# Performance work log

Hardware: AMD Instinct MI355X
Metric: run time of the kernel (lower is better)

Reference implementation:

```python
import jax, jax.numpy as jnp
import numpy as np

N, E, H = 4096, 32768, 8
D0, C1, C2, C3 = 256, 448, 384, 256
K, M, G = 4, 500, 2000
NEG = 0.2   # GATConv LeakyReLU negative slope
EPS = 1e-5  # LayerNorm eps


def _gat(x, src, dst, W, a_s, a_d, b, heads, out_ch, concat):
    # PyG GATConv (self-loops already appended to src/dst by caller).
    n = x.shape[0]
    xp = (x @ W).reshape(n, heads, out_ch)                 # [N,H,C]
    s = jnp.einsum('nhc,hc->nh', xp, a_s)                  # alpha_src per node
    d = jnp.einsum('nhc,hc->nh', xp, a_d)                  # alpha_dst per node
    e = jax.nn.leaky_relu(s[src] + d[dst], NEG)            # [E,H]
    m = jax.ops.segment_max(e, dst, num_segments=n)
    m = jnp.where(jnp.isfinite(m), m, 0.0)
    p = jnp.exp(e - m[dst])
    z = jax.ops.segment_sum(p, dst, num_segments=n)
    alpha = p / (z[dst] + 1e-16)                           # per-dst softmax
    out = jax.ops.segment_sum(alpha[:, :, None] * xp[src], dst, num_segments=n)
    out = out.reshape(n, heads * out_ch) if concat else out[:, 0, :]
    return out + b


def _ln(x, g, b):
    mu = x.mean(-1, keepdims=True)
    v = ((x - mu) ** 2).mean(-1, keepdims=True)
    return (x - mu) * jax.lax.rsqrt(v + EPS) * g + b


def setup_inputs() -> dict:
    key = jax.random.key(0)
    ks = jax.random.split(key, 20)
    sc = 0.05
    inp = {
        'x': jax.random.normal(ks[0], (N, D0), jnp.float32),
        'edge_index': jax.random.randint(ks[1], (2, E), 0, N, jnp.int32),
        'W1': jax.random.normal(ks[2], (D0, H * C1), jnp.float32) * sc,
        'as1': jax.random.normal(ks[3], (H, C1), jnp.float32) * sc,
        'ad1': jax.random.normal(ks[4], (H, C1), jnp.float32) * sc,
        'b1': jnp.zeros((H * C1,), jnp.float32),
        'g1': jnp.ones((H * C1,), jnp.float32),
        'be1': jnp.zeros((H * C1,), jnp.float32),
        'W2': jax.random.normal(ks[5], (H * C1, H * C2), jnp.float32) * sc,
        'as2': jax.random.normal(ks[6], (H, C2), jnp.float32) * sc,
        'ad2': jax.random.normal(ks[7], (H, C2), jnp.float32) * sc,
        'b2': jnp.zeros((H * C2,), jnp.float32),
        'g2': jnp.ones((H * C2,), jnp.float32),
        'be2': jnp.zeros((H * C2,), jnp.float32),
        'W3': jax.random.normal(ks[8], (H * C2, H * C3), jnp.float32) * sc,
        'as3': jax.random.normal(ks[9], (H, C3), jnp.float32) * sc,
        'ad3': jax.random.normal(ks[10], (H, C3), jnp.float32) * sc,
        'b3': jnp.zeros((H * C3,), jnp.float32),
        'g3': jnp.ones((H * C3,), jnp.float32),
        'be3': jnp.zeros((H * C3,), jnp.float32),
        'Wh': jax.random.normal(ks[11], (K, H * C3, M), jnp.float32) * sc,
        'ash': jax.random.normal(ks[12], (K, 1, M), jnp.float32) * sc,
        'adh': jax.random.normal(ks[13], (K, 1, M), jnp.float32) * sc,
        'bh': jnp.zeros((K, M), jnp.float32),
        'idx': jnp.arange(G, dtype=jnp.int32).reshape(K, M),
    }
    return inp


def reference(x, edge_index, W1, as1, ad1, b1, g1, be1, W2, as2, ad2, b2, g2, be2,
              W3, as3, ad3, b3, g3, be3, Wh, ash, adh, bh, idx):
    n = x.shape[0]
    # eval mode: dropout_edge is identity; PyG GATConv adds self-loops
    loops = jnp.arange(n, dtype=edge_index.dtype)
    src = jnp.concatenate([edge_index[0], loops])
    dst = jnp.concatenate([edge_index[1], loops])

    h = jax.nn.relu(_gat(x, src, dst, W1, as1, ad1, b1, H, C1, True))
    h = _ln(h, g1, be1)
    h = jax.nn.relu(_gat(h, src, dst, W2, as2, ad2, b2, H, C2, True))
    h = _ln(h, g2, be2)
    h = jax.nn.relu(_gat(h, src, dst, W3, as3, ad3, b3, H, C3, True))
    h = _ln(h, g3, be3)

    per_head = jax.vmap(
        lambda Wk, ak_s, ak_d, bk: _gat(h, src, dst, Wk, ak_s, ak_d, bk, 1, M, False)
    )(Wh, ash, adh, bh)                                    # [K,N,M]

    vals = per_head.transpose(1, 0, 2).reshape(n, K * M)   # [N, G] in head order
    full = jnp.zeros((n, G), vals.dtype).at[:, idx.reshape(-1)].set(vals)
    return full, per_head
```

## Files before the change

### kernel.cpp

```cpp
#include <hip/hip_runtime.h>

#define NN 4096
#define EE 32768
#define ETOT (EE + NN)
#define HH 8
#define KK 4
#define MM 500
#define GG 2000
#define NEGS 0.2f
#define LNEPS 1e-5f

typedef unsigned short ushort;
typedef _Float16 half_t;
typedef __attribute__((ext_vector_type(8))) _Float16 half8;
typedef __attribute__((ext_vector_type(4))) _Float16 half4;
typedef __attribute__((ext_vector_type(4))) float floatx4;


__device__ __forceinline__ void get_edge(const int* __restrict__ ei, int e, int& s, int& d) {
    if (e < EE) { s = ei[e]; d = ei[EE + e]; }
    else        { s = e - EE; d = e - EE; }
}

__device__ __forceinline__ half_t f2h(float x) { return (half_t)x; }

__device__ __forceinline__ void async_lds16(const half_t* g, half_t* l) {
    __builtin_amdgcn_global_load_lds(
        (const __attribute__((address_space(1))) unsigned int*)(const void*)g,
        (__attribute__((address_space(3))) unsigned int*)(void*)l,
        16, 0, 0);
}


__global__ void k_count(const int* __restrict__ ei, int* deg) {
    int e = blockIdx.x * 256 + threadIdx.x;
    if (e < ETOT) { int s, d; get_edge(ei, e, s, d); atomicAdd(&deg[d], 1); }
}

__global__ void k_scan(int* deg, int* rs, int n) {
    __shared__ int sums[1024];
    int tid = threadIdx.x;
    int base = tid * 4;
    int loc[4]; int s = 0;
    #pragma unroll
    for (int i = 0; i < 4; i++) {
        int v = (base + i < n) ? deg[base + i] : 0;
        loc[i] = s; s += v;
    }
    #pragma unroll
    for (int i = 0; i < 4; i++)
        if (base + i < n) deg[base + i] = 0;
    sums[tid] = s;
    __syncthreads();
    for (int off = 1; off < 1024; off <<= 1) {
        int v = (tid >= off) ? sums[tid - off] : 0;
        __syncthreads();
        sums[tid] += v;
        __syncthreads();
    }
    int prev = (tid > 0) ? sums[tid - 1] : 0;
    #pragma unroll
    for (int i = 0; i < 4; i++)
        if (base + i < n) rs[base + i] = prev + loc[i];
    if (tid == 1023) rs[n] = sums[1023];
}

__global__ void k_fill_f2h(const int* __restrict__ ei, const int* __restrict__ rs,
                           int* cur, int* csr_src,
                           const floatx4* __restrict__ x4, half4* __restrict__ xh4) {
    int i = blockIdx.x * 256 + threadIdx.x;
    if (i < ETOT) {
        int s, d; get_edge(ei, i, s, d);
        int pos = rs[d] + atomicAdd(&cur[d], 1);
        csr_src[pos] = s;
    }
    if (i < NN * 64) {
        floatx4 v = x4[i];
        half4 o;
        o[0] = f2h(v[0]); o[1] = f2h(v[1]); o[2] = f2h(v[2]); o[3] = f2h(v[3]);
        xh4[i] = o;
    }
}


__device__ __forceinline__ void sd_body(const half_t* __restrict__ xp,
                                        const float* __restrict__ as_,
                                        const float* __restrict__ ad_,
                                        float* s, float* d, int H, int C,
                                        int idx, int lane) {
    const half4* row4 = (const half4*)(xp + (size_t)idx * C);
    int h = idx % H;
    const float* av = as_ + (size_t)h * C;
    const float* bv = ad_ + (size_t)h * C;
    int C4 = C >> 2;
    float ss = 0.f, dd = 0.f;
    for (int c4 = lane; c4 < C4; c4 += 64) {
        half4 v = row4[c4];
        floatx4 a = *(const floatx4*)(av + c4 * 4);
        floatx4 b = *(const floatx4*)(bv + c4 * 4);
        float x0 = (float)v[0], x1 = (float)v[1], x2 = (float)v[2], x3 = (float)v[3];
        ss += x0 * a[0] + x1 * a[1] + x2 * a[2] + x3 * a[3];
        dd += x0 * b[0] + x1 * b[1] + x2 * b[2] + x3 * b[3];
    }
    #pragma unroll
    for (int o = 32; o > 0; o >>= 1) {
        ss += __shfl_down(ss, o, 64);
        dd += __shfl_down(dd, o, 64);
    }
    if (lane == 0) { s[idx] = ss; d[idx] = dd; }
}

__global__ __launch_bounds__(256) void k_sd4(const half_t* __restrict__ xp,
                                             const float* __restrict__ as_,
                                             const float* __restrict__ ad_,
                                             float* s, float* d, int H, int C, int npairs) {
    int idx = blockIdx.x * 4 + (threadIdx.x >> 6);
    if (idx < npairs)
        sd_body(xp, as_, ad_, s, d, H, C, idx, threadIdx.x & 63);
}


__global__ __launch_bounds__(256) void k_sd_wt(
    const half_t* __restrict__ xp, const float* __restrict__ as_,
    const float* __restrict__ ad_, float* s, float* d, int H, int C, int nsd, int npairs,
    const float* __restrict__ W, half_t* __restrict__ Wt,
    int Kd, int Nvalid, int ldw, long long sW, long long sWt, int wgx, int wgy) {
    __shared__ float t[32][33];
    int bid = blockIdx.x;
    if (bid < nsd) {
        int idx = bid * 4 + (threadIdx.x >> 6);
        if (idx < npairs)
            sd_body(xp, as_, ad_, s, d, H, C, idx, threadIdx.x & 63);
        return;
    }
    int wb = bid - nsd;
    int bx = wb % wgx;
    int rem = wb / wgx;
    int by = rem % wgy;
    int bz = rem / wgy;
    const float* Wp = W + (size_t)bz * sW;
    half_t* Wtp = Wt + (size_t)bz * sWt;
    int n0 = bx * 32, k0 = by * 32;
    int tx = threadIdx.x & 31, ty = threadIdx.x >> 5;
    #pragma unroll
    for (int i = 0; i < 32; i += 8)
        t[ty + i][tx] = (n0 + tx < Nvalid) ? Wp[(size_t)(k0 + ty + i) * ldw + n0 + tx] : 0.f;
    __syncthreads();
    #pragma unroll
    for (int i = 0; i < 32; i += 8)
        Wtp[(size_t)(n0 + ty + i) * Kd + k0 + tx] = f2h(t[tx][ty + i]);
}


__global__ __launch_bounds__(256) void k_wt(const float* __restrict__ W,
                                            half_t* __restrict__ Wt,
                                            int Kd, int Nvalid, int ldw,
                                            long long sW, long long sWt) {
    __shared__ float t[32][33];
    const float* Wp = W + (size_t)blockIdx.z * sW;
    half_t* Wtp = Wt + (size_t)blockIdx.z * sWt;
    int n0 = blockIdx.x * 32, k0 = blockIdx.y * 32;
    int tx = threadIdx.x & 31, ty = threadIdx.x >> 5;
    #pragma unroll
    for (int i = 0; i < 32; i += 8)
        t[ty + i][tx] = (n0 + tx < Nvalid) ? Wp[(size_t)(k0 + ty + i) * ldw + n0 + tx] : 0.f;
    __syncthreads();
    #pragma unroll
    for (int i = 0; i < 32; i += 8)
        Wtp[(size_t)(n0 + ty + i) * Kd + k0 + tx] = f2h(t[tx][ty + i]);
}


#define BM 128
#define BN 128
#define BK 64

__global__ __launch_bounds__(256) void k_gemm_mfma(
    const half_t* __restrict__ A,
    const half_t* __restrict__ Bt,
    half_t* __restrict__ C,
    int Kd, int Nreal, int ldc,
    long long strideBt, long long strideC)
{
    __shared__ __align__(16) half_t As[BM * BK];
    __shared__ __align__(16) half_t Bs[BN * BK];

    const half_t* Btp = Bt + (size_t)blockIdx.z * strideBt;
    half_t* Cp = C + (size_t)blockIdx.z * strideC;
    int col0 = blockIdx.x * BN, row0 = blockIdx.y * BM;

    int lane = threadIdx.x & 63;
    int wave = threadIdx.x >> 6;
    int wm = (wave >> 1) * 64, wn = (wave & 1) * 64;

    int srow = wave * 32 + (lane >> 3);
    int gchunk = (lane & 7) ^ ((lane >> 3) & 7);
    const half_t* ga = A   + (size_t)(row0 + srow) * Kd + gchunk * 8;
    const half_t* gb = Btp + (size_t)(col0 + srow) * Kd + gchunk * 8;
    half_t* lA = &As[(wave * 32) * BK];
    half_t* lB = &Bs[(wave * 32) * BK];

    int r = lane & 15;
    int rx = r & 7;

    floatx4 acc[4][4];
    #pragma unroll
    for (int i = 0; i < 4; i++)
        #pragma unroll
        for (int j = 0; j < 4; j++) acc[i][j] = (floatx4){0.f, 0.f, 0.f, 0.f};

    for (int k0 = 0; k0 < Kd; k0 += BK) {
        #pragma unroll
        for (int j = 0; j < 4; j++) {
            async_lds16(ga + k0 + (size_t)(j * 8) * Kd, lA + (j * 8) * BK);
            async_lds16(gb + k0 + (size_t)(j * 8) * Kd, lB + (j * 8) * BK);
        }
        __syncthreads();
        #pragma unroll
        for (int kk = 0; kk < BK; kk += 32) {
            int phys = (((kk >> 3) + (lane >> 4)) ^ rx) << 3;
            half8 a[4], b[4];
            #pragma unroll
            for (int i = 0; i < 4; i++)
                a[i] = *(const half8*)&As[(wm + i * 16 + r) * BK + phys];
            #pragma unroll
            for (int j = 0; j < 4; j++)
                b[j] = *(const half8*)&Bs[(wn + j * 16 + r) * BK + phys];
            #pragma unroll
            for (int i = 0; i < 4; i++)
                #pragma unroll
                for (int j = 0; j < 4; j++)
                    acc[i][j] = __builtin_amdgcn_mfma_f32_16x16x32_f16(a[i], b[j], acc[i][j], 0, 0, 0);
        }
        __syncthreads();
    }

    int q4 = (lane >> 4) * 4;
    #pragma unroll
    for (int i = 0; i < 4; i++) {
        #pragma unroll
        for (int rr = 0; rr < 4; rr++) {
            int row = row0 + wm + i * 16 + q4 + rr;
            #pragma unroll
            for (int j = 0; j < 4; j++) {
                int col = col0 + wn + j * 16 + (lane & 15);
                if (col < Nreal) Cp[(size_t)row * ldc + col] = f2h(acc[i][j][rr]);
            }
        }
    }
}


__global__ __launch_bounds__(256) void k_agg_ln(
    const half_t* __restrict__ xp, const float* __restrict__ s, const float* __restrict__ d,
    const int* __restrict__ csr_src, const int* __restrict__ rs,
    const float* __restrict__ bias, const float* __restrict__ gam,
    const float* __restrict__ bet, half_t* __restrict__ outh, int H, int C) {
    __shared__ int sh_src[256];
    __shared__ float sh_w[256 * HH];
    __shared__ float sh_d[HH];
    __shared__ float sh_z[HH];
    __shared__ float red[256];
    __shared__ float red2[256];
    int n = blockIdx.x, tid = threadIdx.x;
    int Dout = H * C;
    int NCH = Dout >> 3;
    int CCH = C >> 3;
    int start = rs[n], end = rs[n + 1];
    if (tid < H) { sh_d[tid] = d[(size_t)n * H + tid]; sh_z[tid] = 0.f; }
    float acc[2][8];
    #pragma unroll
    for (int a = 0; a < 2; a++)
        #pragma unroll
        for (int e = 0; e < 8; e++) acc[a][e] = 0.f;

    for (int e0 = start; e0 < end; e0 += 256) {
        int cnt = min(256, end - e0);
        if (tid < cnt) sh_src[tid] = csr_src[e0 + tid];
        __syncthreads();
        for (int i = tid; i < cnt * H; i += 256) {
            int ei = i / H, h = i - ei * H;
            float v = s[(size_t)sh_src[ei] * H + h] + sh_d[h];
            v = (v >= 0.f) ? v : NEGS * v;
            sh_w[i] = expf(v);
        }
        __syncthreads();
        if (tid < H) {
            float zz = 0.f;
            for (int i = 0; i < cnt; i++) zz += sh_w[i * H + tid];
            sh_z[tid] += zz;
        }
        int ai = 0;
        for (int ch = tid; ch < NCH; ch += 256, ai++) {
            int h = ch / CCH;
            float a0 = acc[ai][0], a1 = acc[ai][1], a2 = acc[ai][2], a3 = acc[ai][3];
            float a4 = acc[ai][4], a5 = acc[ai][5], a6 = acc[ai][6], a7 = acc[ai][7];
            for (int i = 0; i < cnt; i++) {
                float w = sh_w[i * H + h];
                half8 v = *(const half8*)(xp + (size_t)sh_src[i] * Dout + (ch << 3));
                a0 += w * (float)v[0]; a1 += w * (float)v[1];
                a2 += w * (float)v[2]; a3 += w * (float)v[3];
                a4 += w * (float)v[4]; a5 += w * (float)v[5];
                a6 += w * (float)v[6]; a7 += w * (float)v[7];
            }
            acc[ai][0] = a0; acc[ai][1] = a1; acc[ai][2] = a2; acc[ai][3] = a3;
            acc[ai][4] = a4; acc[ai][5] = a5; acc[ai][6] = a6; acc[ai][7] = a7;
        }
        __syncthreads();
    }

    float vals[2][8];
    float sum = 0.f, sumsq = 0.f;
    int ai = 0;
    for (int ch = tid; ch < NCH; ch += 256, ai++) {
        int h = ch / CCH;
        float zi = 1.f / (sh_z[h] + 1e-16f);
        #pragma unroll
        for (int e = 0; e < 8; e++) {
            float v = acc[ai][e] * zi + bias[(ch << 3) + e];
            v = fmaxf(v, 0.f);
            vals[ai][e] = v;
            sum += v; sumsq += v * v;
        }
    }
    red[tid] = sum; red2[tid] = sumsq;
    __syncthreads();
    for (int o = 128; o > 0; o >>= 1) {
        if (tid < o) { red[tid] += red[tid + o]; red2[tid] += red2[tid + o]; }
        __syncthreads();
    }
    float mu = red[0] / Dout;
    float var = red2[0] / Dout - mu * mu;
    float rstd = rsqrtf(var + LNEPS);
    ai = 0;
    for (int ch = tid; ch < NCH; ch += 256, ai++) {
        half8 o;
        #pragma unroll
        for (int e = 0; e < 8; e++)
            o[e] = f2h((vals[ai][e] - mu) * rstd * gam[(ch << 3) + e] + bet[(ch << 3) + e]);
        *(half8*)(outh + (size_t)n * Dout + (ch << 3)) = o;
    }
}


__global__ __launch_bounds__(256) void k_agg_head(
    const half_t* __restrict__ xp, const float* __restrict__ s, const float* __restrict__ d,
    const int* __restrict__ csr_src, const int* __restrict__ rs,
    const float* __restrict__ bias, const int* __restrict__ idxm,
    float* out_full, float* out_ph) {
    __shared__ int sh_src[256];
    __shared__ float sh_w[256 * KK];
    __shared__ float sh_d[KK];
    __shared__ float sh_z[KK];
    int n = blockIdx.x, tid = threadIdx.x;
    const int Dout = KK * MM;
    const int NCH = Dout >> 3;
    int start = rs[n], end = rs[n + 1];
    if (tid < KK) { sh_d[tid] = d[(size_t)n * KK + tid]; sh_z[tid] = 0.f; }
    float acc[8];
    #pragma unroll
    for (int e = 0; e < 8; e++) acc[e] = 0.f;
    int ch = tid;
    int cb = ch << 3;

    for (int e0 = start; e0 < end; e0 += 256) {
        int cnt = min(256, end - e0);
        if (tid < cnt) sh_src[tid] = csr_src[e0 + tid];
        __syncthreads();
        for (int i = tid; i < cnt * KK; i += 256) {
            int ei = i / KK, k = i - ei * KK;
            float v = s[(size_t)sh_src[ei] * KK + k] + sh_d[k];
            v = (v >= 0.f) ? v : NEGS * v;
            sh_w[i] = expf(v);
        }
        __syncthreads();
        if (tid < KK) {
            float zz = 0.f;
            for (int i = 0; i < cnt; i++) zz += sh_w[i * KK + tid];
            sh_z[tid] += zz;
        }
        if (ch < NCH) {
            for (int i = 0; i < cnt; i++) {
                const float* wv = &sh_w[i * KK];
                half8 v = *(const half8*)(xp + (size_t)sh_src[i] * Dout + cb);
                #pragma unroll
                for (int e = 0; e < 8; e++)
                    acc[e] += wv[(cb + e) / MM] * (float)v[e];
            }
        }
        __syncthreads();
    }
    if (ch < NCH) {
        #pragma unroll
        for (int e = 0; e < 8; e++) {
            int c = cb + e;
            int k = c / MM, m = c - k * MM;
            float v = acc[e] / (sh_z[k] + 1e-16f) + bias[c];
            out_ph[((size_t)k * NN + n) * MM + m] = v;
            out_full[(size_t)n * GG + idxm[c]] = v;
        }
    }
}


extern "C" void kernel_launch(void* const* d_in, const int* in_sizes, int n_in,
                              void* d_out, int out_size, void* d_ws, size_t ws_size,
                              hipStream_t stream) {
    (void)in_sizes; (void)n_in; (void)out_size; (void)ws_size;
    const float* x   = (const float*)d_in[0];
    const int*   ei  = (const int*)d_in[1];
    const float* W1  = (const float*)d_in[2];
    const float* as1 = (const float*)d_in[3];
    const float* ad1 = (const float*)d_in[4];
    const float* b1  = (const float*)d_in[5];
    const float* g1  = (const float*)d_in[6];
    const float* be1 = (const float*)d_in[7];
    const float* W2  = (const float*)d_in[8];
    const float* as2 = (const float*)d_in[9];
    const float* ad2 = (const float*)d_in[10];
    const float* b2  = (const float*)d_in[11];
    const float* g2  = (const float*)d_in[12];
    const float* be2 = (const float*)d_in[13];
    const float* W3  = (const float*)d_in[14];
    const float* as3 = (const float*)d_in[15];
    const float* ad3 = (const float*)d_in[16];
    const float* b3  = (const float*)d_in[17];
    const float* g3  = (const float*)d_in[18];
    const float* be3 = (const float*)d_in[19];
    const float* Wh  = (const float*)d_in[20];
    const float* ash = (const float*)d_in[21];
    const float* adh = (const float*)d_in[22];
    const float* bh  = (const float*)d_in[23];
    const int*   idxm = (const int*)d_in[24];
    float* out = (float*)d_out;

    char* w = (char*)d_ws;
    auto carve = [&](size_t bytes) { char* p = w; w += (bytes + 255) & ~(size_t)255; return p; };
    half_t* xp16    = (half_t*)carve((size_t)NN * 3584 * 2);
    half_t* Wt      = (half_t*)carve((size_t)3072 * 3584 * 2);
    float*  sarr    = (float*)carve((size_t)NN * HH * 4);
    float*  darr    = (float*)carve((size_t)NN * HH * 4);
    int*    csr_src = (int*)carve((size_t)ETOT * 4);
    int*    rowst   = (int*)carve((size_t)(NN + 1) * 4);
    int*    cur     = (int*)carve((size_t)NN * 4);
    half_t* Ah = (half_t*)d_out;

    hipMemsetAsync(cur, 0, (size_t)NN * 4, stream);
    k_count<<<(ETOT + 255) / 256, 256, 0, stream>>>(ei, cur);
    k_scan<<<1, 1024, 0, stream>>>(cur, rowst, NN);
    k_fill_f2h<<<(NN * 64 + 255) / 256, 256, 0, stream>>>(
        ei, rowst, cur, csr_src, (const floatx4*)x, (half4*)Ah);

    k_wt<<<dim3(3584 / 32, 256 / 32, 1), 256, 0, stream>>>(W1, Wt, 256, 3584, 3584, 0, 0);
    k_gemm_mfma<<<dim3(3584 / BN, NN / BM, 1), 256, 0, stream>>>(
        Ah, Wt, xp16, 256, 3584, 3584, 0, 0);
    k_sd_wt<<<8192 + 10752, 256, 0, stream>>>(
        xp16, as1, ad1, sarr, darr, HH, 448, 8192, NN * HH,
        W2, Wt, 3584, 3072, 3072, 0, 0, 96, 112);
    k_agg_ln<<<NN, 256, 0, stream>>>(xp16, sarr, darr, csr_src, rowst,
                                     b1, g1, be1, Ah, HH, 448);

    k_gemm_mfma<<<dim3(3072 / BN, NN / BM, 1), 256, 0, stream>>>(
        Ah, Wt, xp16, 3584, 3072, 3072, 0, 0);
    k_sd_wt<<<8192 + 6144, 256, 0, stream>>>(
        xp16, as2, ad2, sarr, darr, HH, 384, 8192, NN * HH,
        W3, Wt, 3072, 2048, 2048, 0, 0, 64, 96);
    k_agg_ln<<<NN, 256, 0, stream>>>(xp16, sarr, darr, csr_src, rowst,
                                     b2, g2, be2, Ah, HH, 384);

    k_gemm_mfma<<<dim3(2048 / BN, NN / BM, 1), 256, 0, stream>>>(
        Ah, Wt, xp16, 3072, 2048, 2048, 0, 0);
    k_sd_wt<<<8192 + 4096, 256, 0, stream>>>(
        xp16, as3, ad3, sarr, darr, HH, 256, 8192, NN * HH,
        Wh, Wt, 2048, MM, MM, (long long)2048 * MM, (long long)512 * 2048, 16, 64);
    k_agg_ln<<<NN, 256, 0, stream>>>(xp16, sarr, darr, csr_src, rowst,
                                     b3, g3, be3, Ah, HH, 256);

    k_gemm_mfma<<<dim3(512 / BN, NN / BM, KK), 256, 0, stream>>>(
        Ah, Wt, xp16, 2048, MM, GG, (long long)512 * 2048, (long long)MM);
    k_sd4<<<(NN * KK) / 4, 256, 0, stream>>>(xp16, ash, adh, sarr, darr, KK, MM, NN * KK);
    k_agg_head<<<NN, 256, 0, stream>>>(xp16, sarr, darr, csr_src, rowst,
                                       bh, idxm, out, out + (size_t)NN * GG);
}
```

Measured before the change: 644.5 us.

## Reorder layer-1 GAT to aggregate 256-dim inputs before projection

Measured after the change: 745.0 us. +15.6%, slower.

```diff
diff --git a/kernel.cpp b/kernel.cpp
--- a/kernel.cpp
+++ b/kernel.cpp
@@ -79,6 +79,146 @@
         half4 o;
         o[0] = f2h(v[0]); o[1] = f2h(v[1]); o[2] = f2h(v[2]); o[3] = f2h(v[3]);
         xh4[i] = o;
+    }
+}
+
+
+__global__ __launch_bounds__(256) void k_wa(const half_t* __restrict__ Wt1,
+                                            const float* __restrict__ as_,
+                                            const float* __restrict__ ad_,
+                                            float* was, float* wad, int C, int Kd) {
+    int h = blockIdx.x, k = threadIdx.x;
+    const half_t* base = Wt1 + (size_t)h * C * Kd;
+    const float* av = as_ + (size_t)h * C;
+    const float* bv = ad_ + (size_t)h * C;
+    float ss = 0.f, dd = 0.f;
+    for (int c = 0; c < C; c++) {
+        float w = (float)base[(size_t)c * Kd + k];
+        ss += w * av[c];
+        dd += w * bv[c];
+    }
+    was[h * Kd + k] = ss;
+    wad[h * Kd + k] = dd;
+}
+
+
+__global__ __launch_bounds__(256) void k_sd_x(const float* __restrict__ x,
+                                              const float* __restrict__ was,
+                                              const float* __restrict__ wad,
+                                              float* s, float* d) {
+    int n = blockIdx.x * 4 + (threadIdx.x >> 6);
+    int lane = threadIdx.x & 63;
+    const float* xr = x + (size_t)n * 256;
+    float x0 = xr[lane], x1 = xr[lane + 64], x2 = xr[lane + 128], x3 = xr[lane + 192];
+    #pragma unroll
+    for (int h = 0; h < HH; h++) {
+        const float* ws = was + h * 256;
+        const float* wd = wad + h * 256;
+        float ss = x0 * ws[lane] + x1 * ws[lane + 64] + x2 * ws[lane + 128] + x3 * ws[lane + 192];
+        float dd = x0 * wd[lane] + x1 * wd[lane + 64] + x2 * wd[lane + 128] + x3 * wd[lane + 192];
+        #pragma unroll
+        for (int o = 32; o > 0; o >>= 1) {
+            ss += __shfl_down(ss, o, 64);
+            dd += __shfl_down(dd, o, 64);
+        }
+        if (lane == 0) { s[n * HH + h] = ss; d[n * HH + h] = dd; }
+    }
+}
+
+
+__global__ __launch_bounds__(256) void k_agg_x(
+    const half_t* __restrict__ xh, const float* __restrict__ s, const float* __restrict__ d,
+    const int* __restrict__ csr_src, const int* __restrict__ rs,
+    half_t* __restrict__ aggx) {
+    __shared__ half_t sx[16][256];
+    __shared__ int ssrc[16];
+    __shared__ float sw[16][HH];
+    __shared__ float sh_d[HH];
+    __shared__ float sh_z[HH];
+    int n = blockIdx.x, tid = threadIdx.x;
+    int h = tid >> 5, kc = (tid & 31) * 8;
+    if (tid < HH) { sh_d[tid] = d[(size_t)n * HH + tid]; sh_z[tid] = 0.f; }
+    float acc[8];
+    #pragma unroll
+    for (int e = 0; e < 8; e++) acc[e] = 0.f;
+    int start = rs[n], end = rs[n + 1];
+
+    for (int e0 = start; e0 < end; e0 += 16) {
+        int cnt = min(16, end - e0);
+        if (tid < cnt) ssrc[tid] = csr_src[e0 + tid];
+        __syncthreads();
+        for (int q = tid; q < cnt * 32; q += 256) {
+            int er = q >> 5, ec = q & 31;
+            *((half8*)&sx[er][0] + ec) = *((const half8*)(xh + (size_t)ssrc[er] * 256) + ec);
+        }
+        if (tid < cnt * HH) {
+            int er = tid >> 3, hh = tid & 7;
+            float v = s[(size_t)ssrc[er] * HH + hh] + sh_d[hh];
+            v = (v >= 0.f) ? v : NEGS * v;
+            sw[er][hh] = expf(v);
+        }
+        __syncthreads();
+        if (tid < HH) {
+            float zz = 0.f;
+            for (int i = 0; i < cnt; i++) zz += sw[i][tid];
+            sh_z[tid] += zz;
+        }
+        for (int i = 0; i < cnt; i++) {
+            float w = sw[i][h];
+            half8 v = *(const half8*)&sx[i][kc];
+            acc[0] += w * (float)v[0]; acc[1] += w * (float)v[1];
+            acc[2] += w * (float)v[2]; acc[3] += w * (float)v[3];
+            acc[4] += w * (float)v[4]; acc[5] += w * (float)v[5];
+            acc[6] += w * (float)v[6]; acc[7] += w * (float)v[7];
+        }
+    }
+    __syncthreads();
+    float zi = 1.f / (sh_z[h] + 1e-16f);
+    half8 o;
+    #pragma unroll
+    for (int e = 0; e < 8; e++) o[e] = f2h(acc[e] * zi);
+    *(half8*)(aggx + (size_t)n * (HH * 256) + h * 256 + kc) = o;
+}
+
+
+__global__ __launch_bounds__(256) void k_ln(const half_t* __restrict__ xin,
+                                            const float* __restrict__ bias,
+                                            const float* __restrict__ gam,
+                                            const float* __restrict__ bet,
+                                            half_t* __restrict__ outh, int Dout) {
+    __shared__ float red[256];
+    __shared__ float red2[256];
+    int n = blockIdx.x, tid = threadIdx.x;
+    int NCH = Dout >> 3;
+    float vals[2][8];
+    float sum = 0.f, sumsq = 0.f;
+    int ai = 0;
+    for (int ch = tid; ch < NCH; ch += 256, ai++) {
+        half8 v = *(const half8*)(xin + (size_t)n * Dout + (ch << 3));
+        #pragma unroll
+        for (int e = 0; e < 8; e++) {
+            float val = (float)v[e] + bias[(ch << 3) + e];
+            val = fmaxf(val, 0.f);
+            vals[ai][e] = val;
+            sum += val; sumsq += val * val;
+        }
+    }
+    red[tid] = sum; red2[tid] = sumsq;
+    __syncthreads();
+    for (int o = 128; o > 0; o >>= 1) {
+        if (tid < o) { red[tid] += red[tid + o]; red2[tid] += red2[tid + o]; }
+        __syncthreads();
+    }
+    float mu = red[0] / Dout;
+    float var = red2[0] / Dout - mu * mu;
+    float rstd = rsqrtf(var + LNEPS);
+    ai = 0;
+    for (int ch = tid; ch < NCH; ch += 256, ai++) {
+        half8 o;
+        #pragma unroll
+        for (int e = 0; e < 8; e++)
+            o[e] = f2h((vals[ai][e] - mu) * rstd * gam[(ch << 3) + e] + bet[(ch << 3) + e]);
+        *(half8*)(outh + (size_t)n * Dout + (ch << 3)) = o;
     }
 }
 
@@ -179,12 +319,13 @@
     const half_t* __restrict__ A,
     const half_t* __restrict__ Bt,
     half_t* __restrict__ C,
-    int Kd, int Nreal, int ldc,
-    long long strideBt, long long strideC)
+    int Kd, int lda, int Nreal, int ldc,
+    long long strideA, long long strideBt, long long strideC)
 {
     __shared__ __align__(16) half_t As[BM * BK];
     __shared__ __align__(16) half_t Bs[BN * BK];
 
+    const half_t* Ap  = A  + (size_t)blockIdx.z * strideA;
     const half_t* Btp = Bt + (size_t)blockIdx.z * strideBt;
     half_t* Cp = C + (size_t)blockIdx.z * strideC;
     int col0 = blockIdx.x * BN, row0 = blockIdx.y * BM;
@@ -195,7 +336,7 @@
 
     int srow = wave * 32 + (lane >> 3);
     int gchunk = (lane & 7) ^ ((lane >> 3) & 7);
-    const half_t* ga = A   + (size_t)(row0 + srow) * Kd + gchunk * 8;
+    const half_t* ga = Ap  + (size_t)(row0 + srow) * lda + gchunk * 8;
     const half_t* gb = Btp + (size_t)(col0 + srow) * Kd + gchunk * 8;
     half_t* lA = &As[(wave * 32) * BK];
     half_t* lB = &Bs[(wave * 32) * BK];
@@ -212,7 +353,7 @@
     for (int k0 = 0; k0 < Kd; k0 += BK) {
         #pragma unroll
         for (int j = 0; j < 4; j++) {
-            async_lds16(ga + k0 + (size_t)(j * 8) * Kd, lA + (j * 8) * BK);
+            async_lds16(ga + k0 + (size_t)(j * 8) * lda, lA + (j * 8) * BK);
             async_lds16(gb + k0 + (size_t)(j * 8) * Kd, lB + (j * 8) * BK);
         }
         __syncthreads();
@@ -437,13 +578,17 @@
     char* w = (char*)d_ws;
     auto carve = [&](size_t bytes) { char* p = w; w += (bytes + 255) & ~(size_t)255; return p; };
     half_t* xp16    = (half_t*)carve((size_t)NN * 3584 * 2);
-    half_t* Wt      = (half_t*)carve((size_t)3072 * 3584 * 2);
+    half_t* Wt      = (half_t*)carve((size_t)12100000 * 2);
     float*  sarr    = (float*)carve((size_t)NN * HH * 4);
     float*  darr    = (float*)carve((size_t)NN * HH * 4);
+    float*  was     = (float*)carve((size_t)HH * 256 * 4);
+    float*  wad     = (float*)carve((size_t)HH * 256 * 4);
     int*    csr_src = (int*)carve((size_t)ETOT * 4);
     int*    rowst   = (int*)carve((size_t)(NN + 1) * 4);
     int*    cur     = (int*)carve((size_t)NN * 4);
-    half_t* Ah = (half_t*)d_out;
+    half_t* Ah   = (half_t*)d_out;
+    half_t* aggx = (half_t*)(out + (size_t)NN * GG);
+    half_t* Wt2  = Wt + (size_t)1048576;
 
     hipMemsetAsync(cur, 0, (size_t)NN * 4, stream);
     k_count<<<(ETOT + 255) / 256, 256, 0, stream>>>(ei, cur);
@@ -452,16 +597,17 @@
         ei, rowst, cur, csr_src, (const floatx4*)x, (half4*)Ah);
 
     k_wt<<<dim3(3584 / 32, 256 / 32, 1), 256, 0, stream>>>(W1, Wt, 256, 3584, 3584, 0, 0);
-    k_gemm_mfma<<<dim3(3584 / BN, NN / BM, 1), 256, 0, stream>>>(
-        Ah, Wt, xp16, 256, 3584, 3584, 0, 0);
-    k_sd_wt<<<8192 + 10752, 256, 0, stream>>>(
-        xp16, as1, ad1, sarr, darr, HH, 448, 8192, NN * HH,
-        W2, Wt, 3584, 3072, 3072, 0, 0, 96, 112);
-    k_agg_ln<<<NN, 256, 0, stream>>>(xp16, sarr, darr, csr_src, rowst,
-                                     b1, g1, be1, Ah, HH, 448);
-
+    k_wa<<<HH, 256, 0, stream>>>(Wt, as1, ad1, was, wad, 448, 256);
+    k_sd_x<<<NN / 4, 256, 0, stream>>>(x, was, wad, sarr, darr);
+    k_agg_x<<<NN, 256, 0, stream>>>(Ah, sarr, darr, csr_src, rowst, aggx);
+    k_gemm_mfma<<<dim3(4, NN / BM, HH), 256, 0, stream>>>(
+        aggx, Wt, xp16, 256, HH * 256, 448, 3584,
+        256LL, (long long)448 * 256, 448LL);
+    k_ln<<<NN, 256, 0, stream>>>(xp16, b1, g1, be1, Ah, 3584);
+
+    k_wt<<<dim3(3072 / 32, 3584 / 32, 1), 256, 0, stream>>>(W2, Wt2, 3584, 3072, 3072, 0, 0);
     k_gemm_mfma<<<dim3(3072 / BN, NN / BM, 1), 256, 0, stream>>>(
-        Ah, Wt, xp16, 3584, 3072, 3072, 0, 0);
+        Ah, Wt2, xp16, 3584, 3584, 3072, 3072, 0, 0, 0);
     k_sd_wt<<<8192 + 6144, 256, 0, stream>>>(
         xp16, as2, ad2, sarr, darr, HH, 384, 8192, NN * HH,
         W3, Wt, 3072, 2048, 2048, 0, 0, 64, 96);
@@ -469,7 +615,7 @@
                                      b2, g2, be2, Ah, HH, 384);
 
     k_gemm_mfma<<<dim3(2048 / BN, NN / BM, 1), 256, 0, stream>>>(
-        Ah, Wt, xp16, 3072, 2048, 2048, 0, 0);
+        Ah, Wt, xp16, 3072, 3072, 2048, 2048, 0, 0, 0);
     k_sd_wt<<<8192 + 4096, 256, 0, stream>>>(
         xp16, as3, ad3, sarr, darr, HH, 256, 8192, NN * HH,
         Wh, Wt, 2048, MM, MM, (long long)2048 * MM, (long long)512 * 2048, 16, 64);
@@ -477,7 +623,7 @@
                                      b3, g3, be3, Ah, HH, 256);
 
     k_gemm_mfma<<<dim3(512 / BN, NN / BM, KK), 256, 0, stream>>>(
-        Ah, Wt, xp16, 2048, MM, GG, (long long)512 * 2048, (long long)MM);
+        Ah, Wt, xp16, 2048, 2048, MM, GG, 0, (long long)512 * 2048, (long long)MM);
     k_sd4<<<(NN * KK) / 4, 256, 0, stream>>>(xp16, ash, adh, sarr, darr, KK, MM, NN * KK);
     k_agg_head<<<NN, 256, 0, stream>>>(xp16, sarr, darr, csr_src, rowst,
                                        bh, idxm, out, out + (size_t)NN * GG);
```
